# Optimization experiments

Measured on AMD Instinct MI355X. Metric: run time of the kernel, lower is better.

Reference implementation:

```python
import jax, jax.numpy as jnp
import numpy as np

D_MODEL, N_HEADS, D_FF = 768, 12, 3072
B, S = 2, 2048
EPS = 1e-6

def _ln(x, alpha, bias):
    # Matches torch: std with Bessel correction (unbiased), scalar alpha/bias
    mean = x.mean(axis=-1, keepdims=True)
    std = jnp.std(x, axis=-1, keepdims=True, ddof=1)
    return alpha * (x - mean) / (std + EPS) + bias

def setup_inputs() -> dict:
    key = jax.random.key(0)
    ks = jax.random.split(key, 12)
    def w(k, shp):
        return jax.random.normal(k, shp, dtype=jnp.float32) * 0.02
    inp = {
        "x": jax.random.normal(ks[0], (B, S, D_MODEL), dtype=jnp.float32),
        "mask": jnp.ones((B, 1, 1, S), dtype=jnp.int32),
        "wq": w(ks[1], (D_MODEL, D_MODEL)), "bq": jnp.zeros((D_MODEL,), jnp.float32),
        "wk": w(ks[2], (D_MODEL, D_MODEL)), "bk": jnp.zeros((D_MODEL,), jnp.float32),
        "wv": w(ks[3], (D_MODEL, D_MODEL)), "bv": jnp.zeros((D_MODEL,), jnp.float32),
        "wo": w(ks[4], (D_MODEL, D_MODEL)), "bo": jnp.zeros((D_MODEL,), jnp.float32),
        "w1": w(ks[5], (D_MODEL, D_FF)), "b1": jnp.zeros((D_FF,), jnp.float32),
        "w2": w(ks[6], (D_FF, D_MODEL)), "b2": jnp.zeros((D_MODEL,), jnp.float32),
        "ln1_a": jnp.ones((1,), jnp.float32), "ln1_b": jnp.zeros((1,), jnp.float32),
        "ln2_a": jnp.ones((1,), jnp.float32), "ln2_b": jnp.zeros((1,), jnp.float32),
    }
    return inp

def reference(x, mask, wq, bq, wk, bk, wv, bv, wo, bo, w1, b1, w2, b2,
              ln1_a, ln1_b, ln2_a, ln2_b):
    d_k = D_MODEL // N_HEADS
    # --- residual 1: pre-LN self-attention ---
    h = _ln(x, ln1_a, ln1_b)
    q = (h @ wq + bq).reshape(B, S, N_HEADS, d_k).transpose(0, 2, 1, 3)
    k = (h @ wk + bk).reshape(B, S, N_HEADS, d_k).transpose(0, 2, 1, 3)
    v = (h @ wv + bv).reshape(B, S, N_HEADS, d_k).transpose(0, 2, 1, 3)
    scores = jnp.einsum('bhqd,bhkd->bhqk', q, k) / jnp.sqrt(jnp.float32(d_k))
    scores = jnp.where(mask == 0, jnp.float32(-1e9), scores)
    attn = jax.nn.softmax(scores, axis=-1)            # [B,H,S,S] materialized, as in source
    ctx = jnp.einsum('bhqk,bhkd->bhqd', attn, v)
    ctx = ctx.transpose(0, 2, 1, 3).reshape(B, S, D_MODEL)
    x = x + (ctx @ wo + bo)
    # --- residual 2: pre-LN FFN ---
    h = _ln(x, ln2_a, ln2_b)
    ffn = jax.nn.relu(h @ w1 + b1) @ w2 + b2
    return x + ffn
```

## Files before the change

kernel.cpp:

```cpp
#include <hip/hip_runtime.h>
#include <math.h>

#define DM    768
#define NH    12
#define DKH   64
#define DFF   3072
#define BATCH 2
#define SLEN  2048
#define MTOT  4096
#define LNEPS 1e-6f
#define QSCALE 0.18033688011112042f

typedef unsigned short u16;
typedef __attribute__((ext_vector_type(8))) short bf16x8;
typedef __attribute__((ext_vector_type(4))) float f32x4;
typedef __attribute__((ext_vector_type(4))) unsigned short us4;

__device__ __forceinline__ u16 f2bf(float f) {
    union { float f; unsigned int u; } v; v.f = f;
    unsigned int r = v.u + 0x7FFFu + ((v.u >> 16) & 1u);
    return (u16)(r >> 16);
}

__device__ __forceinline__ unsigned pk2bf_t(float lo, float hi) {
    union { float f; unsigned u; } a, b;
    a.f = lo; b.f = hi;
    return __builtin_amdgcn_perm(b.u, a.u, 0x07060302u);
}

__device__ __forceinline__ void gld16(const void* g, void* lds) {
    __builtin_amdgcn_global_load_lds(
        (const __attribute__((address_space(1))) unsigned int*)(unsigned long long)g,
        (__attribute__((address_space(3))) unsigned int*)(unsigned int)(unsigned long long)lds,
        16, 0, 0);
}

__global__ __launch_bounds__(256) void ln_kernel(const float* __restrict__ x,
                                                 u16* __restrict__ out,
                                                 const float* __restrict__ alpha_p,
                                                 const float* __restrict__ beta_p,
                                                 const float* __restrict__ b2,
                                                 float* __restrict__ out2) {
    int row = blockIdx.x;
    const float* xr = x + (size_t)row * DM;
    int t = threadIdx.x;
    float v0 = xr[t], v1 = xr[t + 256], v2 = xr[t + 512];
    float s = v0 + v1 + v2;
    #pragma unroll
    for (int off = 32; off > 0; off >>= 1) s += __shfl_down(s, off);
    __shared__ float red[4], red2[4];
    int wv = t >> 6, ln = t & 63;
    if (ln == 0) red[wv] = s;
    __syncthreads();
    float mean = (red[0] + red[1] + red[2] + red[3]) * (1.0f / 768.0f);
    float d0 = v0 - mean, d1 = v1 - mean, d2 = v2 - mean;
    float sq = d0 * d0 + d1 * d1 + d2 * d2;
    #pragma unroll
    for (int off = 32; off > 0; off >>= 1) sq += __shfl_down(sq, off);
    if (ln == 0) red2[wv] = sq;
    __syncthreads();
    float var = (red2[0] + red2[1] + red2[2] + red2[3]) * (1.0f / 767.0f);
    float scale = alpha_p[0] / (sqrtf(var) + LNEPS);
    float bias = beta_p[0];
    u16* orow = out + (size_t)row * DM;
    orow[t]       = f2bf(d0 * scale + bias);
    orow[t + 256] = f2bf(d1 * scale + bias);
    orow[t + 512] = f2bf(d2 * scale + bias);
    if (out2) {
        float* o2 = out2 + (size_t)row * DM;
        o2[t]       = v0 + b2[t];
        o2[t + 256] = v1 + b2[t + 256];
        o2[t + 512] = v2 + b2[t + 512];
    }
}

__global__ __launch_bounds__(256) void wcast_all(
        const float* __restrict__ wq, const float* __restrict__ wk,
        const float* __restrict__ wv, const float* __restrict__ wo,
        const float* __restrict__ w1, const float* __restrict__ w2,
        u16* __restrict__ wqT, u16* __restrict__ wkT, u16* __restrict__ wvT,
        u16* __restrict__ woT, u16* __restrict__ w1T, u16* __restrict__ w2T) {
    __shared__ float tile[32][33];
    int bid = blockIdx.x;
    const float* src; u16* dst; int R, C, bx, by;
    if (bid < 2304) {
        int j = bid / 576, tix = bid % 576;
        R = 768; C = 768; bx = tix % 24; by = tix / 24;
        src = (j == 0) ? wq : (j == 1) ? wk : (j == 2) ? wv : wo;
        dst = (j == 0) ? wqT : (j == 1) ? wkT : (j == 2) ? wvT : woT;
    } else if (bid < 4608) {
        int tix = bid - 2304;
        R = 768; C = 3072; bx = tix % 96; by = tix / 96;
        src = w1; dst = w1T;
    } else {
        int tix = bid - 4608;
        R = 3072; C = 768; bx = tix % 24; by = tix / 24;
        src = w2; dst = w2T;
    }
    int t = threadIdx.x, tx = t & 31, ty = t >> 5;
    int r0 = by * 32, c0 = bx * 32;
    #pragma unroll
    for (int p = 0; p < 4; p++)
        tile[ty + p * 8][tx] = src[(size_t)(r0 + ty + p * 8) * C + c0 + tx];
    __syncthreads();
    #pragma unroll
    for (int p = 0; p < 4; p++)
        dst[(size_t)(c0 + ty + p * 8) * R + r0 + tx] = f2bf(tile[tx][ty + p * 8]);
}

template<int EPI>
__device__ __forceinline__ void gemm128_core(const u16* __restrict__ A,
                                             const u16* __restrict__ Wt,
                                             const float* __restrict__ bias,
                                             const float* __restrict__ resid,
                                             void* __restrict__ Cout,
                                             int M, int N, int Kstride, int Kloop,
                                             float scale, int bm, int bn) {
    __shared__ __align__(16) u16 As[2][128 * 32];
    __shared__ __align__(16) u16 Bs[2][128 * 32];
    int t = threadIdx.x;
    int ln = t & 63, w = t >> 6;
    int wm = w >> 1, wn = w & 1;
    int quad = ln >> 4, col = ln & 15;
    int m0 = bm * 128, n0 = bn * 128;

    f32x4 acc[4][4];
    const f32x4 zero = {0.f, 0.f, 0.f, 0.f};
    #pragma unroll
    for (int i = 0; i < 4; i++)
        #pragma unroll
        for (int j = 0; j < 4; j++) acc[i][j] = zero;

    int st_ch = (((ln & 3) ^ ((ln >> 3) & 3))) * 8;
    const u16* Ag = A  + (size_t)(m0 + 32 * w + (ln >> 2)) * Kstride + st_ch;
    const u16* Bg = Wt + (size_t)(n0 + 32 * w + (ln >> 2)) * Kstride + st_ch;

    gld16(Ag,                As[0] + w * 1024);
    gld16(Ag + 16 * Kstride, As[0] + w * 1024 + 512);
    gld16(Bg,                Bs[0] + w * 1024);
    gld16(Bg + 16 * Kstride, Bs[0] + w * 1024 + 512);
    __syncthreads();

    int rch = (quad ^ ((col >> 1) & 3)) * 8;

    for (int k0 = 0; k0 < Kloop; k0 += 32) {
        int cur = (k0 >> 5) & 1, nxt = cur ^ 1;
        if (k0 + 32 < Kloop) {
            gld16(Ag + k0 + 32,                As[nxt] + w * 1024);
            gld16(Ag + k0 + 32 + 16 * Kstride, As[nxt] + w * 1024 + 512);
            gld16(Bg + k0 + 32,                Bs[nxt] + w * 1024);
            gld16(Bg + k0 + 32 + 16 * Kstride, Bs[nxt] + w * 1024 + 512);
        }
        bf16x8 af[4], bfr[4];
        #pragma unroll
        for (int i = 0; i < 4; i++)
            af[i] = *(const bf16x8*)&As[cur][(wm * 64 + i * 16 + col) * 32 + rch];
        #pragma unroll
        for (int j = 0; j < 4; j++)
            bfr[j] = *(const bf16x8*)&Bs[cur][(wn * 64 + j * 16 + col) * 32 + rch];
        #pragma unroll
        for (int i = 0; i < 4; i++)
            #pragma unroll
            for (int j = 0; j < 4; j++)
                acc[i][j] = __builtin_amdgcn_mfma_f32_16x16x32_bf16(af[i], bfr[j], acc[i][j], 0, 0, 0);
        __syncthreads();
    }

    #pragma unroll
    for (int i = 0; i < 4; i++) {
        int mb = m0 + wm * 64 + i * 16 + quad * 4;
        #pragma unroll
        for (int j = 0; j < 4; j++) {
            int n = n0 + wn * 64 + j * 16 + col;
            if (EPI == 0 || EPI == 1) {
                float bs = bias[n];
                u16* Cb = (u16*)Cout;
                #pragma unroll
                for (int r = 0; r < 4; r++) {
                    float f = (acc[i][j][r] + bs) * ((EPI == 0) ? scale : 1.0f);
                    if (EPI == 1) f = fmaxf(f, 0.f);
                    Cb[(size_t)(mb + r) * N + n] = f2bf(f);
                }
            } else if (EPI == 2) {
                float bs = bias[n];
                float* Cf = (float*)Cout;
                #pragma unroll
                for (int r = 0; r < 4; r++)
                    Cf[(size_t)(mb + r) * N + n] =
                        acc[i][j][r] + bs + resid[(size_t)(mb + r) * N + n];
            } else if (EPI == 3) {
                float bs = bias[n];
                u16* Cb = (u16*)Cout;
                us4 pk;
                #pragma unroll
                for (int r = 0; r < 4; r++) pk[r] = f2bf(acc[i][j][r] + bs);
                *(us4*)&Cb[(size_t)n * M + mb] = pk;
            } else {
                float* Cf = (float*)Cout;
                #pragma unroll
                for (int r = 0; r < 4; r++)
                    atomicAdd(&Cf[(size_t)(mb + r) * N + n], acc[i][j][r]);
            }
        }
    }
}

template<int EPI>
__global__ __launch_bounds__(256) void gemm_kernel(const u16* __restrict__ A,
                                                   const u16* __restrict__ Wt,
                                                   const float* __restrict__ bias,
                                                   const float* __restrict__ resid,
                                                   void* __restrict__ C,
                                                   int M, int N, int Kstride, int Kloop,
                                                   float scale) {
    const u16* Az = A  + (size_t)blockIdx.z * Kloop;
    const u16* Wz = Wt + (size_t)blockIdx.z * Kloop;
    gemm128_core<EPI>(Az, Wz, bias, resid, C, M, N, Kstride, Kloop, scale,
                      blockIdx.y, blockIdx.x);
}

__global__ __launch_bounds__(256) void qkv_kernel(const u16* __restrict__ h,
        const u16* __restrict__ wqT, const u16* __restrict__ wkT, const u16* __restrict__ wvT,
        const float* __restrict__ bq, const float* __restrict__ bk, const float* __restrict__ bv,
        u16* __restrict__ q, u16* __restrict__ k, u16* __restrict__ vT) {
    int z = blockIdx.z;
    if (z == 0)      gemm128_core<0>(h, wqT, bq, nullptr, q,  MTOT, DM, DM, DM, QSCALE, blockIdx.y, blockIdx.x);
    else if (z == 1) gemm128_core<0>(h, wkT, bk, nullptr, k,  MTOT, DM, DM, DM, 1.0f,   blockIdx.y, blockIdx.x);
    else             gemm128_core<3>(h, wvT, bv, nullptr, vT, MTOT, DM, DM, DM, 1.0f,   blockIdx.y, blockIdx.x);
}

template<int EPI>
__global__ __launch_bounds__(256) void gemm64_kernel(const u16* __restrict__ A,
                                                     const u16* __restrict__ Wt,
                                                     const float* __restrict__ bias,
                                                     const float* __restrict__ resid,
                                                     void* __restrict__ Cout,
                                                     int M, int N, int Kstride, int Kloop) {
    __shared__ __align__(16) u16 As[2][64 * 32];
    __shared__ __align__(16) u16 Bs[2][64 * 32];
    int t = threadIdx.x, ln = t & 63, w = t >> 6;
    int wm = w >> 1, wn = w & 1;
    int quad = ln >> 4, col = ln & 15;
    int m0 = blockIdx.y * 64, n0 = blockIdx.x * 64;

    f32x4 acc[2][2];
    const f32x4 zero = {0.f, 0.f, 0.f, 0.f};
    #pragma unroll
    for (int i = 0; i < 2; i++)
        #pragma unroll
        for (int j = 0; j < 2; j++) acc[i][j] = zero;

    int st_ch = (((ln & 3) ^ ((ln >> 3) & 3))) * 8;
    const u16* Ag = A  + (size_t)(m0 + 16 * w + (ln >> 2)) * Kstride + st_ch;
    const u16* Bg = Wt + (size_t)(n0 + 16 * w + (ln >> 2)) * Kstride + st_ch;
    gld16(Ag, As[0] + w * 512);
    gld16(Bg, Bs[0] + w * 512);
    __syncthreads();

    int rch = (quad ^ ((col >> 1) & 3)) * 8;

    for (int k0 = 0; k0 < Kloop; k0 += 32) {
        int cur = (k0 >> 5) & 1, nxt = cur ^ 1;
        if (k0 + 32 < Kloop) {
            gld16(Ag + k0 + 32, As[nxt] + w * 512);
            gld16(Bg + k0 + 32, Bs[nxt] + w * 512);
        }
        bf16x8 af[2], bfr[2];
        #pragma unroll
        for (int i = 0; i < 2; i++)
            af[i] = *(const bf16x8*)&As[cur][(wm * 32 + i * 16 + col) * 32 + rch];
        #pragma unroll
        for (int j = 0; j < 2; j++)
            bfr[j] = *(const bf16x8*)&Bs[cur][(wn * 32 + j * 16 + col) * 32 + rch];
        #pragma unroll
        for (int i = 0; i < 2; i++)
            #pragma unroll
            for (int j = 0; j < 2; j++)
                acc[i][j] = __builtin_amdgcn_mfma_f32_16x16x32_bf16(af[i], bfr[j], acc[i][j], 0, 0, 0);
        __syncthreads();
    }

    #pragma unroll
    for (int i = 0; i < 2; i++) {
        int mb = m0 + wm * 32 + i * 16 + quad * 4;
        #pragma unroll
        for (int j = 0; j < 2; j++) {
            int n = n0 + wn * 32 + j * 16 + col;
            float bs = bias[n];
            float* Cf = (float*)Cout;
            #pragma unroll
            for (int r = 0; r < 4; r++)
                Cf[(size_t)(mb + r) * N + n] =
                    acc[i][j][r] + bs + resid[(size_t)(mb + r) * N + n];
        }
    }
}

__global__ __launch_bounds__(256) void attn_kernel(const u16* __restrict__ qg,
                                                   const u16* __restrict__ kg,
                                                   const u16* __restrict__ vTg,
                                                   const int* __restrict__ mask,
                                                   u16* __restrict__ ctx) {
    __shared__ __align__(16) u16 Qs[64 * 64];
    __shared__ __align__(16) u16 KV[4][64 * 64];
    __shared__ __align__(16) u16 Ps[4][32 * 40];
    __shared__ __align__(16) float Msf[2][64];
    __shared__ float Lp[64][2];
    int t = threadIdx.x, ln = t & 63, w = t >> 6;
    int quad = ln >> 4, col = ln & 15;
    int qh = w >> 1, kh = w & 1;
    int bh = blockIdx.x, qb = blockIdx.y;
    int b = bh / NH, h = bh - b * NH;
    int q0 = qb * 64;
    size_t qkbase = ((size_t)b * SLEN) * DM + h * DKH;
    size_t vbase  = ((size_t)h * DKH) * MTOT + (size_t)b * SLEN;

    int sw_st = (((ln & 7) ^ (ln >> 3)) * 8);

    {
        const u16* g0 = qg + qkbase + (size_t)(q0 + 16 * w + (ln >> 3)) * DM + sw_st;
        gld16(g0,          Qs + w * 1024);
        gld16(g0 + 8 * DM, Qs + w * 1024 + 512);
        const u16* kg0 = kg + qkbase + (size_t)(16 * w + (ln >> 3)) * DM + sw_st;
        gld16(kg0,          KV[0] + w * 1024);
        gld16(kg0 + 8 * DM, KV[0] + w * 1024 + 512);
        const u16* vg0 = vTg + vbase + (size_t)(16 * w + (ln >> 3)) * MTOT + sw_st;
        gld16(vg0,            KV[2] + w * 1024);
        gld16(vg0 + 8 * MTOT, KV[2] + w * 1024 + 512);
        if (t < 64) Msf[0][t] = mask[b * SLEN + t] ? 0.f : -1e9f;
    }
    __syncthreads();

    bf16x8 bqf[2][2];
    #pragma unroll
    for (int qgi = 0; qgi < 2; qgi++) {
        int rq = qh * 32 + qgi * 16 + col;
        int cq = ((quad ^ (rq & 7)) * 8);
        bqf[qgi][0] = *(const bf16x8*)&Qs[rq * 64 + cq];
        bqf[qgi][1] = *(const bf16x8*)&Qs[rq * 64 + (cq ^ 32)];
    }

    const u16* kpn = kg + qkbase + (size_t)(64 + 16 * w + (ln >> 3)) * DM + sw_st;
    const u16* vpn = vTg + vbase + (size_t)(16 * w + (ln >> 3)) * MTOT + 64 + sw_st;
    const int* mpn = mask + b * SLEN + 64 + t;

    float lacc[2] = {0.f, 0.f};
    f32x4 Ov[2][4];
    const f32x4 zero = {0.f, 0.f, 0.f, 0.f};
    #pragma unroll
    for (int qgi = 0; qgi < 2; qgi++)
        #pragma unroll
        for (int dg = 0; dg < 4; dg++) Ov[qgi][dg] = zero;
    u16* Psw = &Ps[w][0];

    for (int j0 = 0; j0 < SLEN; j0 += 64) {
        int cur = (j0 >> 6) & 1, nxt = cur ^ 1;
        if (j0 + 64 < SLEN) {
            gld16(kpn,            KV[nxt] + w * 1024);
            gld16(kpn + 8 * DM,   KV[nxt] + w * 1024 + 512);
            gld16(vpn,            KV[2 + nxt] + w * 1024);
            gld16(vpn + 8 * MTOT, KV[2 + nxt] + w * 1024 + 512);
            if (t < 64) Msf[nxt][t] = *mpn ? 0.f : -1e9f;
            kpn += 64 * DM; vpn += 64; mpn += 64;
        }

        bf16x8 ak[2][2];
        #pragma unroll
        for (int kgi = 0; kgi < 2; kgi++) {
            int rk = kh * 32 + kgi * 16 + col;
            int ck = ((quad ^ (rk & 7)) * 8);
            ak[kgi][0] = *(const bf16x8*)&KV[cur][rk * 64 + ck];
            ak[kgi][1] = *(const bf16x8*)&KV[cur][rk * 64 + (ck ^ 32)];
        }
        #pragma unroll
        for (int kgi = 0; kgi < 2; kgi++) {
            f32x4 bias4 = *(const f32x4*)&Msf[cur][kh * 32 + kgi * 16 + quad * 4];
            #pragma unroll
            for (int qgi = 0; qgi < 2; qgi++) {
                f32x4 S = __builtin_amdgcn_mfma_f32_16x16x32_bf16(ak[kgi][0], bqf[qgi][0], bias4, 0, 0, 0);
                S       = __builtin_amdgcn_mfma_f32_16x16x32_bf16(ak[kgi][1], bqf[qgi][1], S,     0, 0, 0);
                float p0 = exp2f(S[0]), p1 = exp2f(S[1]);
                float p2 = exp2f(S[2]), p3 = exp2f(S[3]);
                lacc[qgi] += (p0 + p1) + (p2 + p3);
                uint2 pk;
                pk.x = pk2bf_t(p0, p1);
                pk.y = pk2bf_t(p2, p3);
                *(uint2*)&Psw[(qgi * 16 + col) * 40 + kgi * 16 + quad * 4] = pk;
            }
        }
        bf16x8 ap[2];
        #pragma unroll
        for (int qgi = 0; qgi < 2; qgi++)
            ap[qgi] = *(const bf16x8*)&Psw[(qgi * 16 + col) * 40 + quad * 8];
        #pragma unroll
        for (int dg = 0; dg < 4; dg++) {
            int rv = dg * 16 + col;
            int cv = (((kh * 4 + quad) ^ (rv & 7)) * 8);
            bf16x8 bv = *(const bf16x8*)&KV[2 + cur][rv * 64 + cv];
            Ov[0][dg] = __builtin_amdgcn_mfma_f32_16x16x32_bf16(ap[0], bv, Ov[0][dg], 0, 0, 0);
            Ov[1][dg] = __builtin_amdgcn_mfma_f32_16x16x32_bf16(ap[1], bv, Ov[1][dg], 0, 0, 0);
        }
        __syncthreads();
    }

    #pragma unroll
    for (int qgi = 0; qgi < 2; qgi++) {
        lacc[qgi] += __shfl_xor(lacc[qgi], 16);
        lacc[qgi] += __shfl_xor(lacc[qgi], 32);
        if (quad == 0) Lp[qh * 32 + qgi * 16 + col][kh] = lacc[qgi];
    }
    float* Osh = (float*)&KV[0][0];
    if (kh == 1) {
        #pragma unroll
        for (int qgi = 0; qgi < 2; qgi++)
            #pragma unroll
            for (int dg = 0; dg < 4; dg++)
                *(f32x4*)&Osh[(qh * 64 + dg * 16 + col) * 36 + qgi * 16 + quad * 4] = Ov[qgi][dg];
    }
    __syncthreads();
    if (kh == 0) {
        #pragma unroll
        for (int qgi = 0; qgi < 2; qgi++) {
            float linv[4];
            #pragma unroll
            for (int r = 0; r < 4; r++) {
                int ql = qh * 32 + qgi * 16 + quad * 4 + r;
                linv[r] = 1.0f / (Lp[ql][0] + Lp[ql][1]);
            }
            #pragma unroll
            for (int dg = 0; dg < 4; dg++) {
                f32x4 oo = *(const f32x4*)&Osh[(qh * 64 + dg * 16 + col) * 36 + qgi * 16 + quad * 4];
                #pragma unroll
                for (int r = 0; r < 4; r++) {
                    int qrow = q0 + qh * 32 + qgi * 16 + quad * 4 + r;
                    ctx[qkbase + (size_t)qrow * DM + dg * 16 + col] =
                        f2bf((Ov[qgi][dg][r] + oo[r]) * linv[r]);
                }
            }
        }
    }
}

extern "C" void kernel_launch(void* const* d_in, const int* in_sizes, int n_in,
                              void* d_out, int out_size, void* d_ws, size_t ws_size,
                              hipStream_t stream) {
    const float* x    = (const float*)d_in[0];
    const int*   mask = (const int*)d_in[1];
    const float* wq   = (const float*)d_in[2];
    const float* bq   = (const float*)d_in[3];
    const float* wk   = (const float*)d_in[4];
    const float* bk   = (const float*)d_in[5];
    const float* wv   = (const float*)d_in[6];
    const float* bv   = (const float*)d_in[7];
    const float* wo   = (const float*)d_in[8];
    const float* bo   = (const float*)d_in[9];
    const float* w1   = (const float*)d_in[10];
    const float* b1   = (const float*)d_in[11];
    const float* w2   = (const float*)d_in[12];
    const float* b2   = (const float*)d_in[13];
    const float* ln1a = (const float*)d_in[14];
    const float* ln1b = (const float*)d_in[15];
    const float* ln2a = (const float*)d_in[16];
    const float* ln2b = (const float*)d_in[17];
    float* out = (float*)d_out;

    char* w8 = (char*)d_ws;
    u16*   ffn = (u16*)(w8 + 0);
    u16*   q   = (u16*)(w8 + 0);
    u16*   kb  = (u16*)(w8 + 6291456);
    u16*   vT  = (u16*)(w8 + 12582912);
    u16*   ctx = (u16*)(w8 + 18874368);
    u16*   h   = (u16*)(w8 + 25165824);
    float* x1  = (float*)(w8 + 31457280);
    u16*   wqT = (u16*)(w8 + 44040192);
    u16*   wkT = (u16*)(w8 + 45219840);
    u16*   wvT = (u16*)(w8 + 46399488);
    u16*   woT = (u16*)(w8 + 47579136);
    u16*   w1T = (u16*)(w8 + 48758784);
    u16*   w2T = (u16*)(w8 + 53477376);

    wcast_all<<<6912, 256, 0, stream>>>(wq, wk, wv, wo, w1, w2,
                                        wqT, wkT, wvT, woT, w1T, w2T);
    ln_kernel<<<MTOT, 256, 0, stream>>>(x, h, ln1a, ln1b, nullptr, nullptr);
    qkv_kernel<<<dim3(6, 32, 3), 256, 0, stream>>>(h, wqT, wkT, wvT, bq, bk, bv, q, kb, vT);
    attn_kernel<<<dim3(BATCH * NH, SLEN / 64), 256, 0, stream>>>(q, kb, vT, mask, ctx);
    gemm64_kernel<2><<<dim3(12, 64), 256, 0, stream>>>(ctx, woT, bo, x, (void*)x1,
                                                       MTOT, DM, DM, DM);
    ln_kernel<<<MTOT, 256, 0, stream>>>(x1, h, ln2a, ln2b, b2, out);
    gemm_kernel<1><<<dim3(24, 32), 256, 0, stream>>>(h, w1T, b1, nullptr, (void*)ffn,
                                                     MTOT, DFF, DM, DM, 1.0f);
    gemm_kernel<5><<<dim3(6, 32, 2), 256, 0, stream>>>(ffn, w2T, nullptr, nullptr, (void*)out,
                                                       MTOT, DM, DFF, DFF / 2, 1.0f);
}
```

Before: 294.6 us.

## Double attention query tile, compute row sums via MFMA, merge LN1 with weight cast

The attention kernel now processes 128 queries per block instead of 64, so each K/V tile loaded into LDS is reused across twice as many query rows. This halves K/V traffic per query and halves the grid size, at the cost of more registers for accumulators. The softmax denominator is now computed with an extra MFMA against a vector of ones instead of scalar adds and shuffles. The first LayerNorm and the weight cast/transpose are merged into one launch to drop a kernel boundary. Risks are higher register pressure, lower occupancy and fewer blocks to fill the device.

New measurement: 300.6 us. +2.0%, slower.

```diff
diff --git a/kernel.cpp b/kernel.cpp
--- a/kernel.cpp
+++ b/kernel.cpp
@@ -35,13 +35,12 @@
         16, 0, 0);
 }
 
-__global__ __launch_bounds__(256) void ln_kernel(const float* __restrict__ x,
-                                                 u16* __restrict__ out,
-                                                 const float* __restrict__ alpha_p,
-                                                 const float* __restrict__ beta_p,
-                                                 const float* __restrict__ b2,
-                                                 float* __restrict__ out2) {
-    int row = blockIdx.x;
+__device__ __forceinline__ void ln_body(const float* __restrict__ x,
+                                        u16* __restrict__ out,
+                                        const float* __restrict__ alpha_p,
+                                        const float* __restrict__ beta_p,
+                                        const float* __restrict__ b2,
+                                        float* __restrict__ out2, int row) {
     const float* xr = x + (size_t)row * DM;
     int t = threadIdx.x;
     float v0 = xr[t], v1 = xr[t + 256], v2 = xr[t + 512];
@@ -74,14 +73,44 @@
     }
 }
 
-__global__ __launch_bounds__(256) void wcast_all(
+__global__ __launch_bounds__(256) void ln_kernel(const float* __restrict__ x,
+                                                 u16* __restrict__ out,
+                                                 const float* __restrict__ alpha_p,
+                                                 const float* __restrict__ beta_p,
+                                                 const float* __restrict__ b2,
+                                                 float* __restrict__ out2) {
+    ln_body(x, out, alpha_p, beta_p, b2, out2, blockIdx.x);
+}
+
+__device__ __forceinline__ void wcast_body(const float* __restrict__ src,
+                                           u16* __restrict__ dst,
+                                           int R, int C, int bx, int by) {
+    __shared__ float tile[32][33];
+    int t = threadIdx.x, tx = t & 31, ty = t >> 5;
+    int r0 = by * 32, c0 = bx * 32;
+    #pragma unroll
+    for (int p = 0; p < 4; p++)
+        tile[ty + p * 8][tx] = src[(size_t)(r0 + ty + p * 8) * C + c0 + tx];
+    __syncthreads();
+    #pragma unroll
+    for (int p = 0; p < 4; p++)
+        dst[(size_t)(c0 + ty + p * 8) * R + r0 + tx] = f2bf(tile[tx][ty + p * 8]);
+}
+
+__global__ __launch_bounds__(256) void prep_kernel(
+        const float* __restrict__ x, u16* __restrict__ h,
+        const float* __restrict__ ln1a, const float* __restrict__ ln1b,
         const float* __restrict__ wq, const float* __restrict__ wk,
         const float* __restrict__ wv, const float* __restrict__ wo,
         const float* __restrict__ w1, const float* __restrict__ w2,
         u16* __restrict__ wqT, u16* __restrict__ wkT, u16* __restrict__ wvT,
         u16* __restrict__ woT, u16* __restrict__ w1T, u16* __restrict__ w2T) {
-    __shared__ float tile[32][33];
     int bid = blockIdx.x;
+    if (bid < MTOT) {
+        ln_body(x, h, ln1a, ln1b, nullptr, nullptr, bid);
+        return;
+    }
+    bid -= MTOT;
     const float* src; u16* dst; int R, C, bx, by;
     if (bid < 2304) {
         int j = bid / 576, tix = bid % 576;
@@ -97,15 +126,7 @@
         R = 3072; C = 768; bx = tix % 24; by = tix / 24;
         src = w2; dst = w2T;
     }
-    int t = threadIdx.x, tx = t & 31, ty = t >> 5;
-    int r0 = by * 32, c0 = bx * 32;
-    #pragma unroll
-    for (int p = 0; p < 4; p++)
-        tile[ty + p * 8][tx] = src[(size_t)(r0 + ty + p * 8) * C + c0 + tx];
-    __syncthreads();
-    #pragma unroll
-    for (int p = 0; p < 4; p++)
-        dst[(size_t)(c0 + ty + p * 8) * R + r0 + tx] = f2bf(tile[tx][ty + p * 8]);
+    wcast_body(src, dst, R, C, bx, by);
 }
 
 template<int EPI>
@@ -301,26 +322,28 @@
                                                    const u16* __restrict__ vTg,
                                                    const int* __restrict__ mask,
                                                    u16* __restrict__ ctx) {
-    __shared__ __align__(16) u16 Qs[64 * 64];
+    __shared__ __align__(16) u16 Qs[128 * 64];
     __shared__ __align__(16) u16 KV[4][64 * 64];
-    __shared__ __align__(16) u16 Ps[4][32 * 40];
+    __shared__ __align__(16) u16 Ps[4][64 * 40];
     __shared__ __align__(16) float Msf[2][64];
-    __shared__ float Lp[64][2];
+    __shared__ float Lp[128];
     int t = threadIdx.x, ln = t & 63, w = t >> 6;
     int quad = ln >> 4, col = ln & 15;
     int qh = w >> 1, kh = w & 1;
     int bh = blockIdx.x, qb = blockIdx.y;
     int b = bh / NH, h = bh - b * NH;
-    int q0 = qb * 64;
+    int q0 = qb * 128;
     size_t qkbase = ((size_t)b * SLEN) * DM + h * DKH;
     size_t vbase  = ((size_t)h * DKH) * MTOT + (size_t)b * SLEN;
 
     int sw_st = (((ln & 7) ^ (ln >> 3)) * 8);
 
     {
-        const u16* g0 = qg + qkbase + (size_t)(q0 + 16 * w + (ln >> 3)) * DM + sw_st;
-        gld16(g0,          Qs + w * 1024);
-        gld16(g0 + 8 * DM, Qs + w * 1024 + 512);
+        const u16* g0 = qg + qkbase + (size_t)(q0 + 32 * w + (ln >> 3)) * DM + sw_st;
+        gld16(g0,           Qs + w * 2048);
+        gld16(g0 + 8 * DM,  Qs + w * 2048 + 512);
+        gld16(g0 + 16 * DM, Qs + w * 2048 + 1024);
+        gld16(g0 + 24 * DM, Qs + w * 2048 + 1536);
         const u16* kg0 = kg + qkbase + (size_t)(16 * w + (ln >> 3)) * DM + sw_st;
         gld16(kg0,          KV[0] + w * 1024);
         gld16(kg0 + 8 * DM, KV[0] + w * 1024 + 512);
@@ -331,26 +354,31 @@
     }
     __syncthreads();
 
-    bf16x8 bqf[2][2];
-    #pragma unroll
-    for (int qgi = 0; qgi < 2; qgi++) {
-        int rq = qh * 32 + qgi * 16 + col;
+    bf16x8 bqf[4][2];
+    #pragma unroll
+    for (int qgi = 0; qgi < 4; qgi++) {
+        int rq = qh * 64 + qgi * 16 + col;
         int cq = ((quad ^ (rq & 7)) * 8);
         bqf[qgi][0] = *(const bf16x8*)&Qs[rq * 64 + cq];
         bqf[qgi][1] = *(const bf16x8*)&Qs[rq * 64 + (cq ^ 32)];
     }
 
+    bf16x8 vones;
+    #pragma unroll
+    for (int i = 0; i < 8; i++) vones[i] = (short)0x3F80;
+
     const u16* kpn = kg + qkbase + (size_t)(64 + 16 * w + (ln >> 3)) * DM + sw_st;
     const u16* vpn = vTg + vbase + (size_t)(16 * w + (ln >> 3)) * MTOT + 64 + sw_st;
     const int* mpn = mask + b * SLEN + 64 + t;
 
-    float lacc[2] = {0.f, 0.f};
-    f32x4 Ov[2][4];
+    f32x4 Ov[4][4], Lv[4];
     const f32x4 zero = {0.f, 0.f, 0.f, 0.f};
     #pragma unroll
-    for (int qgi = 0; qgi < 2; qgi++)
+    for (int qgi = 0; qgi < 4; qgi++) {
+        Lv[qgi] = zero;
         #pragma unroll
         for (int dg = 0; dg < 4; dg++) Ov[qgi][dg] = zero;
+    }
     u16* Psw = &Ps[w][0];
 
     for (int j0 = 0; j0 < SLEN; j0 += 64) {
@@ -376,65 +404,69 @@
         for (int kgi = 0; kgi < 2; kgi++) {
             f32x4 bias4 = *(const f32x4*)&Msf[cur][kh * 32 + kgi * 16 + quad * 4];
             #pragma unroll
-            for (int qgi = 0; qgi < 2; qgi++) {
+            for (int qgi = 0; qgi < 4; qgi++) {
                 f32x4 S = __builtin_amdgcn_mfma_f32_16x16x32_bf16(ak[kgi][0], bqf[qgi][0], bias4, 0, 0, 0);
                 S       = __builtin_amdgcn_mfma_f32_16x16x32_bf16(ak[kgi][1], bqf[qgi][1], S,     0, 0, 0);
                 float p0 = exp2f(S[0]), p1 = exp2f(S[1]);
                 float p2 = exp2f(S[2]), p3 = exp2f(S[3]);
-                lacc[qgi] += (p0 + p1) + (p2 + p3);
                 uint2 pk;
                 pk.x = pk2bf_t(p0, p1);
                 pk.y = pk2bf_t(p2, p3);
                 *(uint2*)&Psw[(qgi * 16 + col) * 40 + kgi * 16 + quad * 4] = pk;
             }
         }
-        bf16x8 ap[2];
-        #pragma unroll
-        for (int qgi = 0; qgi < 2; qgi++)
+        bf16x8 ap[4];
+        #pragma unroll
+        for (int qgi = 0; qgi < 4; qgi++) {
             ap[qgi] = *(const bf16x8*)&Psw[(qgi * 16 + col) * 40 + quad * 8];
+            Lv[qgi] = __builtin_amdgcn_mfma_f32_16x16x32_bf16(ap[qgi], vones, Lv[qgi], 0, 0, 0);
+        }
         #pragma unroll
         for (int dg = 0; dg < 4; dg++) {
             int rv = dg * 16 + col;
             int cv = (((kh * 4 + quad) ^ (rv & 7)) * 8);
             bf16x8 bv = *(const bf16x8*)&KV[2 + cur][rv * 64 + cv];
-            Ov[0][dg] = __builtin_amdgcn_mfma_f32_16x16x32_bf16(ap[0], bv, Ov[0][dg], 0, 0, 0);
-            Ov[1][dg] = __builtin_amdgcn_mfma_f32_16x16x32_bf16(ap[1], bv, Ov[1][dg], 0, 0, 0);
+            #pragma unroll
+            for (int qgi = 0; qgi < 4; qgi++)
+                Ov[qgi][dg] = __builtin_amdgcn_mfma_f32_16x16x32_bf16(ap[qgi], bv, Ov[qgi][dg], 0, 0, 0);
         }
         __syncthreads();
     }
 
-    #pragma unroll
-    for (int qgi = 0; qgi < 2; qgi++) {
-        lacc[qgi] += __shfl_xor(lacc[qgi], 16);
-        lacc[qgi] += __shfl_xor(lacc[qgi], 32);
-        if (quad == 0) Lp[qh * 32 + qgi * 16 + col][kh] = lacc[qgi];
-    }
     float* Osh = (float*)&KV[0][0];
     if (kh == 1) {
         #pragma unroll
-        for (int qgi = 0; qgi < 2; qgi++)
+        for (int qgi = 0; qgi < 4; qgi++) {
             #pragma unroll
             for (int dg = 0; dg < 4; dg++)
-                *(f32x4*)&Osh[(qh * 64 + dg * 16 + col) * 36 + qgi * 16 + quad * 4] = Ov[qgi][dg];
+                #pragma unroll
+                for (int r = 0; r < 4; r++)
+                    Osh[(size_t)(qh * 64 + qgi * 16 + quad * 4 + r) * 64 + dg * 16 + col] =
+                        Ov[qgi][dg][r];
+            if (col == 0) {
+                #pragma unroll
+                for (int r = 0; r < 4; r++)
+                    Lp[qh * 64 + qgi * 16 + quad * 4 + r] = Lv[qgi][r];
+            }
+        }
     }
     __syncthreads();
     if (kh == 0) {
         #pragma unroll
-        for (int qgi = 0; qgi < 2; qgi++) {
+        for (int qgi = 0; qgi < 4; qgi++) {
             float linv[4];
             #pragma unroll
             for (int r = 0; r < 4; r++) {
-                int ql = qh * 32 + qgi * 16 + quad * 4 + r;
-                linv[r] = 1.0f / (Lp[ql][0] + Lp[ql][1]);
+                int ql = qh * 64 + qgi * 16 + quad * 4 + r;
+                linv[r] = 1.0f / (Lv[qgi][r] + Lp[ql]);
             }
             #pragma unroll
             for (int dg = 0; dg < 4; dg++) {
-                f32x4 oo = *(const f32x4*)&Osh[(qh * 64 + dg * 16 + col) * 36 + qgi * 16 + quad * 4];
                 #pragma unroll
                 for (int r = 0; r < 4; r++) {
-                    int qrow = q0 + qh * 32 + qgi * 16 + quad * 4 + r;
-                    ctx[qkbase + (size_t)qrow * DM + dg * 16 + col] =
-                        f2bf((Ov[qgi][dg][r] + oo[r]) * linv[r]);
+                    int ql = qh * 64 + qgi * 16 + quad * 4 + r;
+                    float o = Ov[qgi][dg][r] + Osh[(size_t)ql * 64 + dg * 16 + col];
+                    ctx[qkbase + (size_t)(q0 + ql) * DM + dg * 16 + col] = f2bf(o * linv[r]);
                 }
             }
         }
@@ -479,11 +511,11 @@
     u16*   w1T = (u16*)(w8 + 48758784);
     u16*   w2T = (u16*)(w8 + 53477376);
 
-    wcast_all<<<6912, 256, 0, stream>>>(wq, wk, wv, wo, w1, w2,
-                                        wqT, wkT, wvT, woT, w1T, w2T);
-    ln_kernel<<<MTOT, 256, 0, stream>>>(x, h, ln1a, ln1b, nullptr, nullptr);
+    prep_kernel<<<MTOT + 6912, 256, 0, stream>>>(x, h, ln1a, ln1b,
+                                                 wq, wk, wv, wo, w1, w2,
+                                                 wqT, wkT, wvT, woT, w1T, w2T);
     qkv_kernel<<<dim3(6, 32, 3), 256, 0, stream>>>(h, wqT, wkT, wvT, bq, bk, bv, q, kb, vT);
-    attn_kernel<<<dim3(BATCH * NH, SLEN / 64), 256, 0, stream>>>(q, kb, vT, mask, ctx);
+    attn_kernel<<<dim3(BATCH * NH, SLEN / 128), 256, 0, stream>>>(q, kb, vT, mask, ctx);
     gemm64_kernel<2><<<dim3(12, 64), 256, 0, stream>>>(ctx, woT, bo, x, (void*)x1,
                                                        MTOT, DM, DM, DM);
     ln_kernel<<<MTOT, 256, 0, stream>>>(x1, h, ln2a, ln2b, b2, out);
```
